# Performance work log

Measured on AMD Instinct MI355X. Metric: run time of the kernel, lower is better.

Reference implementation:

```python
import jax, jax.numpy as jnp
import numpy as np

PH = PW = 128   # patch size
SH = SW = 64    # stride
H = W = 512     # image size
NH = (H - (PH - SH)) // SH  # 7 patches vertically
NW = (W - (PW - SW)) // SW  # 7 patches horizontally
N, C = 8, 3


def _patch_weight(up, down, left, right):
    # Faithful vectorization of getPatchWeight (nested if/elif per pixel).
    Wl, Hl = PW - SW, PH - SH
    j = np.arange(PW)
    wd = np.where((j < PW - SW) & (not left), j,
         np.where((j > SW) & (not right), PW - j, Wl))
    i = np.arange(PH)
    hd = np.where((i < PH - SH) & (not up), i,
         np.where((i > SH) & (not down), PH - i, Hl))
    return (hd[:, None] * wd[None, :]).astype(np.float32) / float(Wl * Hl)


def _weight_map():
    # [NH, NW, PH, PW] weight per grid position, exact elif order of forward()
    ctr = _patch_weight(0, 0, 0, 0)
    UL = _patch_weight(1, 0, 1, 0); UR = _patch_weight(1, 0, 0, 1)
    DL = _patch_weight(0, 1, 1, 0); DR = _patch_weight(0, 1, 0, 1)
    U = _patch_weight(1, 0, 0, 0); Dw = _patch_weight(0, 1, 0, 0)
    L = _patch_weight(0, 0, 1, 0); R = _patch_weight(0, 0, 0, 1)
    wmap = np.zeros((NH, NW, PH, PW), np.float32)
    for i in range(NH):
        for j in range(NW):
            if i == 0 and j == 0: w = UL
            elif i == 0 and j == NW - 1: w = UR
            elif i == NH - 1 and j == 0: w = DL
            elif i == NH - 1 and j == NW - 1: w = DR
            elif i == 0: w = U
            elif j == 0: w = L
            elif i == NW - 1: w = Dw  # replicates original's numW-based check
            elif j == NW - 1: w = R
            else: w = ctr
            wmap[i, j] = w
    return jnp.asarray(wmap)

_WMAP = _weight_map()


def setup_inputs() -> dict:
    key = jax.random.key(0)
    ks = jax.random.split(key, 8)
    return {
        "inputTensor": jax.random.normal(ks[0], (N, C, H, W), jnp.float32),
        "inputNorm":   jax.random.normal(ks[1], (N, 3, H, W), jnp.float32),
        "W_albedo":  jax.random.normal(ks[2], (3, 6), jnp.float32) * 0.1,
        "b_albedo":  jnp.zeros((3,), jnp.float32),
        "W_normal":  jax.random.normal(ks[3], (3, 6), jnp.float32) * 0.1,
        "b_normal":  jnp.zeros((3,), jnp.float32),
        "W_shading": jax.random.normal(ks[4], (3, 6), jnp.float32) * 0.1,
        "b_shading": jnp.zeros((3,), jnp.float32),
        "W_light":   jax.random.normal(ks[5], (27, 6), jnp.float32) * 0.1,
        "b_light":   jnp.zeros((27,), jnp.float32),
    }


def reference(inputTensor, inputNorm, W_albedo, b_albedo, W_normal, b_normal,
              W_shading, b_shading, W_light, b_light):
    # ---- patch extraction (vectorized unfold) ----
    idx_h = jnp.arange(NH)[:, None] * SH + jnp.arange(PH)[None, :]   # [NH, PH]
    idx_w = jnp.arange(NW)[:, None] * SW + jnp.arange(PW)[None, :]   # [NW, PW]
    # [N, C, NH, NW, PH, PW]
    in_p = inputTensor[:, :, idx_h[:, None, :, None], idx_w[None, :, None, :]]
    nm_p = inputNorm[:, :, idx_h[:, None, :, None], idx_w[None, :, None, :]]
    feat = jnp.concatenate([in_p, nm_p], axis=1)  # [N, 6, NH, NW, PH, PW]

    # ---- stand-in subNetwork: per-pixel 1x1 heads + pooled lighting head ----
    def head(Wm, b):
        return jnp.tanh(jnp.einsum('oc,nchwpq->nohwpq', Wm, feat)
                        + b[None, :, None, None, None, None])

    albedo_p = head(W_albedo, b_albedo)    # [N,3,NH,NW,PH,PW]
    normal_p = head(W_normal, b_normal)
    shading_p = head(W_shading, b_shading)
    pooled = feat.mean(axis=(4, 5))                              # [N,6,NH,NW]
    lighting = jnp.einsum('oc,nchw->nohw', W_light, pooled) \
        + b_light[None, :, None, None]                           # [N,27,NH,NW]

    # ---- weighted overlap-add stitching (vectorized fold) ----
    def stitch(p):
        wp = p * _WMAP[None, None]
        out = jnp.zeros((p.shape[0], 3, H, W), p.dtype)
        return out.at[:, :, idx_h[:, None, :, None],
                      idx_w[None, :, None, :]].add(wp)

    out_albedo = stitch(albedo_p)
    out_normal = stitch(normal_p)
    out_shading = stitch(shading_p)

    # ---- overlap consistency loss on shading (L1 mean per pair, summed) ----
    Wl, Hl = PW - SW, PH - SH
    h_diff = shading_p[:, :, :, 1:, :, :Wl] - shading_p[:, :, :, :-1, :, SW:]
    v_diff = shading_p[:, :, 1:, :, :Hl, :] - shading_p[:, :, :-1, :, SH:, :]
    loss_h = jnp.sum(jnp.abs(h_diff)) / (N * 3 * PH * Wl)
    loss_v = jnp.sum(jnp.abs(v_diff)) / (N * 3 * Hl * PW)
    overlap_loss = (loss_h + loss_v) / (NH * NW)

    return out_albedo, out_normal, out_shading, lighting, overlap_loss
```

## Files before the change

### kernel.cpp

```cpp
#include <hip/hip_runtime.h>

#define NBATCH 8
#define HH 512
#define WW 512
#define NPIX (HH * WW)
#define IMG_ELEMS (NBATCH * 3 * NPIX)
#define OFF_ALBEDO 0
#define OFF_NORMAL ((size_t)IMG_ELEMS)
#define OFF_SHADING ((size_t)(2 * IMG_ELEMS))
#define OFF_LIGHT ((size_t)(3 * IMG_ELEMS))
#define N_LIGHT (NBATCH * 27 * 49)
#define OFF_LOSS (OFF_LIGHT + N_LIGHT)
#define NBLK (NBATCH * 8 * 8 * 2)

typedef float f32x4 __attribute__((ext_vector_type(4)));

__device__ __forceinline__ float fast_tanh(float x) {
    float e = __expf(2.0f * x);
    return 1.0f - 2.0f / (e + 1.0f);
}

__global__ __launch_bounds__(256) void fused_heads_kernel(
    const float* __restrict__ inT, const float* __restrict__ inN,
    const float* __restrict__ Wa, const float* __restrict__ ba,
    const float* __restrict__ Wn, const float* __restrict__ bn,
    const float* __restrict__ Ws, const float* __restrict__ bs,
    float* __restrict__ out, float* __restrict__ P) {
    int bid = blockIdx.x;
    int n = bid >> 7;
    int rem = bid & 127;
    int ti = rem >> 4;
    int rem2 = rem & 15;
    int tj = rem2 >> 1;
    int half = rem2 & 1;

    int t = threadIdx.x;
    int rowc = t >> 4;
    int col4 = t & 15;
    int y = ti * 64 + half * 32 + rowc;
    int x = tj * 64 + col4 * 4;

    f32x4 fa[6], fb[6];
    size_t base0 = ((size_t)(n * 3) * HH + y) * WW + x;
    size_t base1 = base0 + (size_t)16 * WW;
#pragma unroll
    for (int c = 0; c < 3; ++c) {
        fa[c]     = *reinterpret_cast<const f32x4*>(inT + base0 + (size_t)c * NPIX);
        fb[c]     = *reinterpret_cast<const f32x4*>(inT + base1 + (size_t)c * NPIX);
        fa[c + 3] = *reinterpret_cast<const f32x4*>(inN + base0 + (size_t)c * NPIX);
        fb[c + 3] = *reinterpret_cast<const f32x4*>(inN + base1 + (size_t)c * NPIX);
    }

#pragma unroll
    for (int h = 0; h < 3; ++h) {
        const float* W = (h == 0) ? Wa : (h == 1) ? Wn : Ws;
        const float* b = (h == 0) ? ba : (h == 1) ? bn : bs;
        float* o_ptr = out + ((h == 0) ? OFF_ALBEDO : (h == 1) ? OFF_NORMAL : OFF_SHADING);
#pragma unroll
        for (int o = 0; o < 3; ++o) {
            float bv = b[o];
            f32x4 A = {bv, bv, bv, bv};
            f32x4 B = {bv, bv, bv, bv};
#pragma unroll
            for (int c = 0; c < 6; ++c) {
                float w = W[o * 6 + c];
                A.x = fmaf(w, fa[c].x, A.x);
                A.y = fmaf(w, fa[c].y, A.y);
                A.z = fmaf(w, fa[c].z, A.z);
                A.w = fmaf(w, fa[c].w, A.w);
                B.x = fmaf(w, fb[c].x, B.x);
                B.y = fmaf(w, fb[c].y, B.y);
                B.z = fmaf(w, fb[c].z, B.z);
                B.w = fmaf(w, fb[c].w, B.w);
            }
            f32x4 rA = {fast_tanh(A.x), fast_tanh(A.y), fast_tanh(A.z), fast_tanh(A.w)};
            f32x4 rB = {fast_tanh(B.x), fast_tanh(B.y), fast_tanh(B.z), fast_tanh(B.w)};
            *reinterpret_cast<f32x4*>(o_ptr + base0 + (size_t)o * NPIX) = rA;
            *reinterpret_cast<f32x4*>(o_ptr + base1 + (size_t)o * NPIX) = rB;
        }
    }

    float s[6];
#pragma unroll
    for (int c = 0; c < 6; ++c)
        s[c] = (fa[c].x + fa[c].y + fa[c].z + fa[c].w) +
               (fb[c].x + fb[c].y + fb[c].z + fb[c].w);

#pragma unroll
    for (int off = 32; off > 0; off >>= 1) {
#pragma unroll
        for (int c = 0; c < 6; ++c) s[c] += __shfl_down(s[c], off, 64);
    }

    __shared__ float red[4][6];
    int wave = t >> 6;
    int lane = t & 63;
    if (lane == 0) {
#pragma unroll
        for (int c = 0; c < 6; ++c) red[wave][c] = s[c];
    }
    __syncthreads();
    if (t < 6) {
        float v = red[0][t] + red[1][t] + red[2][t] + red[3][t];
        P[(size_t)bid * 8 + t] = v;
    }
}

__global__ __launch_bounds__(256) void lighting_kernel(
    const float* __restrict__ P, const float* __restrict__ Wl,
    const float* __restrict__ bl, float* __restrict__ out) {
    int tid = blockIdx.x * blockDim.x + threadIdx.x;
    if (tid > N_LIGHT) return;
    if (tid == N_LIGHT) {
        out[OFF_LOSS] = 0.0f;
        return;
    }
    int n = tid / (27 * 49);
    int r = tid % (27 * 49);
    int o = r / 49;
    int r2 = r % 49;
    int i = r2 / 7;
    int j = r2 % 7;

    f32x4 s0 = {0.f, 0.f, 0.f, 0.f};
    float s4 = 0.f, s5 = 0.f;
#pragma unroll
    for (int di = 0; di < 2; ++di) {
#pragma unroll
        for (int dj = 0; dj < 2; ++dj) {
            int ti = i + di;
            int tj = j + dj;
#pragma unroll
            for (int hf = 0; hf < 2; ++hf) {
                int b = ((n * 8 + ti) * 8 + tj) * 2 + hf;
                const float* p = P + (size_t)b * 8;
                f32x4 v0 = *reinterpret_cast<const f32x4*>(p);
                f32x4 v1 = *reinterpret_cast<const f32x4*>(p + 4);
                s0 += v0;
                s4 += v1.x;
                s5 += v1.y;
            }
        }
    }
    float acc = bl[o];
    const float inv = 1.0f / 16384.0f;
    acc = fmaf(Wl[o * 6 + 0], s0.x * inv, acc);
    acc = fmaf(Wl[o * 6 + 1], s0.y * inv, acc);
    acc = fmaf(Wl[o * 6 + 2], s0.z * inv, acc);
    acc = fmaf(Wl[o * 6 + 3], s0.w * inv, acc);
    acc = fmaf(Wl[o * 6 + 4], s4 * inv, acc);
    acc = fmaf(Wl[o * 6 + 5], s5 * inv, acc);
    out[OFF_LIGHT + tid] = acc;
}

extern "C" void kernel_launch(void* const* d_in, const int* in_sizes, int n_in,
                              void* d_out, int out_size, void* d_ws, size_t ws_size,
                              hipStream_t stream) {
    const float* inT = (const float*)d_in[0];
    const float* inN = (const float*)d_in[1];
    const float* Wa = (const float*)d_in[2];
    const float* ba = (const float*)d_in[3];
    const float* Wn = (const float*)d_in[4];
    const float* bn = (const float*)d_in[5];
    const float* Ws = (const float*)d_in[6];
    const float* bs = (const float*)d_in[7];
    const float* Wl = (const float*)d_in[8];
    const float* bl = (const float*)d_in[9];
    float* out = (float*)d_out;
    float* P = (float*)d_ws;

    fused_heads_kernel<<<NBLK, 256, 0, stream>>>(
        inT, inN, Wa, ba, Wn, bn, Ws, bs, out, P);

    lighting_kernel<<<(N_LIGHT + 1 + 255) / 256, 256, 0, stream>>>(P, Wl, bl, out);
}
```

Baseline: 28.40 us.

## Remap head kernel blocks to full-width row bands for contiguous loads

Each block now covers a 4-row band spanning the full 512-pixel width instead of a 32x64 tile, so each wavefront reads two full 512-float rows with contiguous 16-byte accesses. The per-block pooling reduction now emits one partial sum per 64-column tile for each band via xor-shuffles within 16-lane groups. The lighting kernel then sums 32 band partials per patch instead of 8 tile partials. The aim is better DRAM/cache streaming, at the cost of more partial sums and more reads in the lighting kernel.

```diff
diff --git a/kernel.cpp b/kernel.cpp
--- a/kernel.cpp
+++ b/kernel.cpp
@@ -11,7 +11,8 @@
 #define OFF_LIGHT ((size_t)(3 * IMG_ELEMS))
 #define N_LIGHT (NBATCH * 27 * 49)
 #define OFF_LOSS (OFF_LIGHT + N_LIGHT)
-#define NBLK (NBATCH * 8 * 8 * 2)
+#define NBAND 128
+#define NBLK (NBATCH * NBAND)
 
 typedef float f32x4 __attribute__((ext_vector_type(4)));
 
@@ -28,21 +29,17 @@
     float* __restrict__ out, float* __restrict__ P) {
     int bid = blockIdx.x;
     int n = bid >> 7;
-    int rem = bid & 127;
-    int ti = rem >> 4;
-    int rem2 = rem & 15;
-    int tj = rem2 >> 1;
-    int half = rem2 & 1;
+    int band = bid & 127;
 
     int t = threadIdx.x;
-    int rowc = t >> 4;
-    int col4 = t & 15;
-    int y = ti * 64 + half * 32 + rowc;
-    int x = tj * 64 + col4 * 4;
+    int half = t >> 7;
+    int cidx = t & 127;
+    int x = cidx * 4;
+    int y0 = band * 4 + half;
 
     f32x4 fa[6], fb[6];
-    size_t base0 = ((size_t)(n * 3) * HH + y) * WW + x;
-    size_t base1 = base0 + (size_t)16 * WW;
+    size_t base0 = ((size_t)(n * 3) * HH + y0) * WW + x;
+    size_t base1 = base0 + (size_t)2 * WW;
 #pragma unroll
     for (int c = 0; c < 3; ++c) {
         fa[c]     = *reinterpret_cast<const f32x4*>(inT + base0 + (size_t)c * NPIX);
@@ -87,22 +84,27 @@
                (fb[c].x + fb[c].y + fb[c].z + fb[c].w);
 
 #pragma unroll
-    for (int off = 32; off > 0; off >>= 1) {
+    for (int off = 1; off <= 8; off <<= 1) {
 #pragma unroll
-        for (int c = 0; c < 6; ++c) s[c] += __shfl_down(s[c], off, 64);
+        for (int c = 0; c < 6; ++c) s[c] += __shfl_xor(s[c], off, 64);
     }
 
-    __shared__ float red[4][6];
+    __shared__ float red[4][4][8];
     int wave = t >> 6;
     int lane = t & 63;
-    if (lane == 0) {
+    int g = lane >> 4;
+    if ((lane & 15) == 0) {
 #pragma unroll
-        for (int c = 0; c < 6; ++c) red[wave][c] = s[c];
+        for (int c = 0; c < 6; ++c) red[wave][g][c] = s[c];
     }
     __syncthreads();
-    if (t < 6) {
-        float v = red[0][t] + red[1][t] + red[2][t] + red[3][t];
-        P[(size_t)bid * 8 + t] = v;
+    if (t < 64) {
+        int tj = t >> 3;
+        int c = t & 7;
+        float v = 0.f;
+        if (c < 6)
+            v = red[tj >> 2][tj & 3][c] + red[(tj >> 2) + 2][tj & 3][c];
+        P[(((size_t)(n * NBAND + band)) * 8 + tj) * 8 + c] = v;
     }
 }
 
@@ -124,23 +126,17 @@
 
     f32x4 s0 = {0.f, 0.f, 0.f, 0.f};
     float s4 = 0.f, s5 = 0.f;
-#pragma unroll
-    for (int di = 0; di < 2; ++di) {
-#pragma unroll
-        for (int dj = 0; dj < 2; ++dj) {
-            int ti = i + di;
-            int tj = j + dj;
-#pragma unroll
-            for (int hf = 0; hf < 2; ++hf) {
-                int b = ((n * 8 + ti) * 8 + tj) * 2 + hf;
-                const float* p = P + (size_t)b * 8;
-                f32x4 v0 = *reinterpret_cast<const f32x4*>(p);
-                f32x4 v1 = *reinterpret_cast<const f32x4*>(p + 4);
-                s0 += v0;
-                s4 += v1.x;
-                s5 += v1.y;
-            }
-        }
+    int band0 = i * 16;
+#pragma unroll 4
+    for (int b = 0; b < 32; ++b) {
+        const float* p = P + (((size_t)(n * NBAND + band0 + b)) * 8 + j) * 8;
+        f32x4 a0 = *reinterpret_cast<const f32x4*>(p);
+        f32x4 a1 = *reinterpret_cast<const f32x4*>(p + 4);
+        f32x4 b0 = *reinterpret_cast<const f32x4*>(p + 8);
+        f32x4 b1 = *reinterpret_cast<const f32x4*>(p + 12);
+        s0 += a0 + b0;
+        s4 += a1.x + b1.x;
+        s5 += a1.y + b1.y;
     }
     float acc = bl[o];
     const float inv = 1.0f / 16384.0f;
```

Measured after the change: 34.31 us. +20.8%, slower.
